# Performance work log

Measured on AMD Instinct MI355X. Metric: run time of the kernel, lower is better.

Reference implementation:

```python
import jax, jax.numpy as jnp
import numpy as np

N_QUBITS = 12
MAX_LAYERS = 21
Q_DEPTH = 20
DIM = 2 ** N_QUBITS  # 4096
Q_DELTA = 0.01


def setup_inputs() -> dict:
    key = jax.random.key(0)
    k1, k2 = jax.random.split(key)
    return {
        "input_features": jax.random.normal(k1, (4096, 2048), dtype=jnp.float32),
        "q_params": Q_DELTA * jax.random.normal(k2, (MAX_LAYERS * N_QUBITS,), dtype=jnp.float32),
    }


def _cnot(state, c, t):
    # state: (B, 2,2,...,2); flip target axis where control bit == 1
    s0, s1 = jnp.split(state, 2, axis=c + 1)
    s1 = jnp.flip(s1, axis=t + 1)
    return jnp.concatenate([s0, s1], axis=c + 1)


def _ry(state, theta, w):
    # real RY rotation: [[cos(t/2), -sin(t/2)], [sin(t/2), cos(t/2)]]
    s0, s1 = jnp.split(state, 2, axis=w + 1)
    c = jnp.cos(theta * 0.5)
    s = jnp.sin(theta * 0.5)
    return jnp.concatenate([c * s0 - s * s1, s * s0 + c * s1], axis=w + 1)


def _entangling_layer(state):
    for i in range(0, N_QUBITS - 1, 2):
        state = _cnot(state, i, i + 1)
    for i in range(1, N_QUBITS - 1, 2):
        state = _cnot(state, i, i + 1)
    return state


def _forward(input_features, q_params):
    q_in = jnp.tanh(input_features) * (np.pi / 2.0)
    B, F = q_in.shape
    # AmplitudeEmbedding: pad with 0.5 to 2^n, then L2-normalize
    padded = jnp.concatenate(
        [q_in, jnp.full((B, DIM - F), 0.5, dtype=q_in.dtype)], axis=1
    )
    state = padded / jnp.linalg.norm(padded, axis=1, keepdims=True)
    state = state.reshape((B,) + (2,) * N_QUBITS)  # qubit 0 = most significant axis

    weights = q_params.reshape(MAX_LAYERS, N_QUBITS)

    @jax.checkpoint
    def layer(st, theta):
        st = _entangling_layer(st)
        for j in range(N_QUBITS):
            st = _ry(st, theta[j], j)
        return st, None

    state, _ = jax.lax.scan(layer, state, weights[1:1 + Q_DEPTH])

    probs = jnp.square(state.reshape(B, DIM))  # (B, 4096)
    bit_pos = N_QUBITS - 1 - jnp.arange(N_QUBITS)
    bits = (jnp.arange(DIM)[:, None] >> bit_pos[None, :]) & 1  # (DIM, 12)
    signs = (1.0 - 2.0 * bits).astype(probs.dtype)
    return probs @ signs  # (B, 12) expvals of PauliZ per qubit


def reference(input_features, q_params):
    return _forward(input_features, q_params)
```

## Files before the change

### kernel.cpp

```cpp
#include <hip/hip_runtime.h>
#include <math.h>

#define LAYERS 20
#define CS_FLOATS 480

typedef float f2 __attribute__((ext_vector_type(2)));

__global__ void cs_precompute(const float* __restrict__ qp, float* __restrict__ cs) {
    int i = threadIdx.x;
    if (i < 240) {
        float t = 0.5f * qp[12 + i];
        cs[2 * i]     = cosf(t);
        cs[2 * i + 1] = sinf(t);
    }
}

#define S0 u0.x
#define S1 u0.y
#define S2 u1.x
#define S3 u1.y
#define S4 u2.x
#define S5 u2.y
#define S6 u3.x
#define S7 u3.y
#define S8 u4.x
#define S9 u4.y
#define S10 u5.x
#define S11 u5.y
#define S12 u6.x
#define S13 u6.y
#define S14 u7.x
#define S15 u7.y
#define S16 u8.x
#define S17 u8.y
#define S18 u9.x
#define S19 u9.y
#define S20 u10.x
#define S21 u10.y
#define S22 u11.x
#define S23 u11.y
#define S24 u12.x
#define S25 u12.y
#define S26 u13.x
#define S27 u13.y
#define S28 u14.x
#define S29 u14.y
#define S30 u15.x
#define S31 u15.y

#define ALL16(F) F(0) F(1) F(2) F(3) F(4) F(5) F(6) F(7) F(8) F(9) F(10) F(11) \
  F(12) F(13) F(14) F(15)
#define ALL32S(F) F(0) F(1) F(2) F(3) F(4) F(5) F(6) F(7) F(8) F(9) F(10) F(11) \
  F(12) F(13) F(14) F(15) F(16) F(17) F(18) F(19) F(20) F(21) F(22) F(23) \
  F(24) F(25) F(26) F(27) F(28) F(29) F(30) F(31)

#define KQ1(F) F(0,8) F(1,9) F(2,10) F(3,11) F(4,12) F(5,13) F(6,14) F(7,15)
#define KQ2(F) F(0,4) F(1,5) F(2,6) F(3,7) F(8,12) F(9,13) F(10,14) F(11,15)
#define KQ3(F) F(0,2) F(1,3) F(4,6) F(5,7) F(8,10) F(9,11) F(12,14) F(13,15)
#define KQ4(F) F(0,1) F(2,3) F(4,5) F(6,7) F(8,9) F(10,11) F(12,13) F(14,15)

#define P16(F) F(0,16) F(1,17) F(2,18) F(3,19) F(4,20) F(5,21) F(6,22) F(7,23) \
  F(8,24) F(9,25) F(10,26) F(11,27) F(12,28) F(13,29) F(14,30) F(15,31)
#define P8(F) F(0,8) F(1,9) F(2,10) F(3,11) F(4,12) F(5,13) F(6,14) F(7,15) \
  F(16,24) F(17,25) F(18,26) F(19,27) F(20,28) F(21,29) F(22,30) F(23,31)
#define P4(F) F(0,4) F(1,5) F(2,6) F(3,7) F(8,12) F(9,13) F(10,14) F(11,15) \
  F(16,20) F(17,21) F(18,22) F(19,23) F(24,28) F(25,29) F(26,30) F(27,31)
#define P2(F) F(0,2) F(1,3) F(4,6) F(5,7) F(8,10) F(9,11) F(12,14) F(13,15) \
  F(16,18) F(17,19) F(20,22) F(21,23) F(24,26) F(25,27) F(28,30) F(29,31)
#define P1(F) F(0,1) F(2,3) F(4,5) F(6,7) F(8,9) F(10,11) F(12,13) F(14,15) \
  F(16,17) F(18,19) F(20,21) F(22,23) F(24,25) F(26,27) F(28,29) F(30,31)

#define XA16(F) F(0) F(1) F(2) F(3) F(4) F(5) F(6) F(7)
#define XB16(F) F(8) F(9) F(10) F(11) F(12) F(13) F(14) F(15)

template <int CTRL>
__device__ __forceinline__ float dppf(float x) {
    return __int_as_float(__builtin_amdgcn_mov_dpp(
        __float_as_int(x), CTRL, 0xF, 0xF, true));
}
template <int IMM>
__device__ __forceinline__ float swzf(float x) {
    return __int_as_float(__builtin_amdgcn_ds_swizzle(__float_as_int(x), IMM));
}

template <bool PRE>
__global__ __launch_bounds__(128)
void qsim(const float* __restrict__ feats,
          const float* __restrict__ qp,
          const float* __restrict__ cs,
          float* __restrict__ out)
{
    __shared__ f2 xch2[2 * 64 * 9];
    float* xchf = (float*)xch2;

    const int tid  = threadIdx.x;
    const int lane = tid & 63;
    const int w    = tid >> 6;
    const int row  = blockIdx.x;

    const int sl0     = lane ^ (lane >> 1) ^ ((lane >> 2) & 5);
    const int addr0   = sl0 << 2;
    const int addr1   = (sl0 ^ 48) << 2;
    const int addrX32 = (lane ^ 32) << 2;

    const int mybase = w * 576 + lane * 9;
    const int pbase  = (1 - w) * 576 + lane * 9;

#define DCLU(k) f2 u##k;
    ALL16(DCLU)
#undef DCLU

    const float* fr = feats + (size_t)row * 2048;
    if (w == 0) {
        float fsum = 0.f;
#define LD(r) { float x_ = tanhf(fr[((r) << 6) + lane]) * 1.5707963267948966f; \
                S##r = x_; fsum += x_ * x_; }
        ALL32S(LD)
#undef LD
#pragma unroll
        for (int m = 32; m >= 1; m >>= 1) fsum += __shfl_xor(fsum, m, 64);
        if (lane == 0) xchf[0] = fsum;
    }
    __syncthreads();
    const float inv = rsqrtf(xchf[0] + 512.0f);
    __syncthreads();
    if (w == 0) {
#define SC(k) u##k *= inv;
        ALL16(SC)
#undef SC
    } else {
        const float padv = 0.5f * inv;
        const f2 pv2 = {padv, padv};
#define PD(k) u##k = pv2;
        ALL16(PD)
#undef PD
    }

#pragma unroll 1
    for (int l = 0; l < LAYERS; ++l) {
        const float* csl = cs + l * 24;

#define BPV(a, x) __int_as_float(__builtin_amdgcn_ds_bpermute( \
                      (((a) & 1) ? addr1 : addr0), __float_as_int(x)))
#define FIX(a) S##a = BPV(a, S##a);
#define C2(a,b) { float t_ = S##a; S##a = BPV(a, S##b); S##b = BPV(b, t_); }
#define C4(a,b,c,d) { float t_ = S##a; S##a = BPV(a, S##b); \
        S##b = BPV(b, S##c); S##c = BPV(c, S##d); S##d = BPV(d, t_); }
#define C8(a,b,c,d,e,f,g,h) { float t_ = S##a; S##a = BPV(a, S##b); \
        S##b = BPV(b, S##c); S##c = BPV(c, S##d); S##d = BPV(d, S##e); \
        S##e = BPV(e, S##f); S##f = BPV(f, S##g); S##g = BPV(g, S##h); \
        S##h = BPV(h, t_); }
        if (w == 0) {
            FIX(0) FIX(1)
            C2(2, 3)
            C4(4, 7, 5, 6)
            C4(8, 12, 11, 14)
            C4(9, 13, 10, 15)
            C8(16, 28, 23, 25, 17, 29, 22, 24)
            C8(18, 31, 21, 26, 19, 30, 20, 27)
        } else {
            C8(0, 16, 12, 27, 2, 19, 14, 24)
            C8(1, 17, 13, 26, 3, 18, 15, 25)
            C8(4, 23, 9, 29, 6, 20, 11, 30)
            C8(5, 22, 8, 28, 7, 21, 10, 31)
        }
#undef BPV
#undef FIX
#undef C2
#undef C4
#undef C8

#define RYPK(a,b) { f2 A_ = u##a, B_ = u##b; \
        u##a = c_ * A_ - s_ * B_; u##b = s_ * A_ + c_ * B_; }
#define RYREGK(J, LIST) { float c_, s_; \
        if constexpr (PRE) { c_ = csl[2*(J)]; s_ = csl[2*(J)+1]; } \
        else { float t_ = 0.5f * qp[12 + l*12 + (J)]; __sincosf(t_, &s_, &c_); } \
        LIST(RYPK) }
        RYREGK(1, KQ1)
        RYREGK(2, KQ2)
        RYREGK(3, KQ3)
        RYREGK(4, KQ4)
#undef RYREGK
#undef RYPK

        {
            float c_, s_;
            if constexpr (PRE) { c_ = csl[10]; s_ = csl[11]; }
            else { float t_ = 0.5f * qp[12 + l*12 + 5]; __sincosf(t_, &s_, &c_); }
            const f2 ss5_ = {-s_, s_};
#define Q5(k) { f2 sw_ = u##k.yx; u##k = c_ * u##k + ss5_ * sw_; }
            ALL16(Q5)
#undef Q5
        }

        {
            float c_, s_, ssel_;
#define GETCS(jj) \
            if constexpr (PRE) { c_ = csl[12 + 2*(jj)]; s_ = csl[13 + 2*(jj)]; } \
            else { float t_ = 0.5f * qp[12 + l*12 + 6 + (jj)]; __sincosf(t_, &s_, &c_); }
#define LQ(k, EX) { f2 p_; p_.x = EX(u##k.x); p_.y = EX(u##k.y); \
                    u##k = c_ * u##k + ssel_ * p_; }

            GETCS(0); ssel_ = (lane & 32) ? s_ : -s_;
#define EX6(x) __int_as_float(__builtin_amdgcn_ds_bpermute(addrX32, __float_as_int(x)))
#define LQ6(k) LQ(k, EX6)
            ALL16(LQ6)
#undef LQ6
#undef EX6
            GETCS(1); ssel_ = (lane & 16) ? s_ : -s_;
#define LQ7(k) LQ(k, swzf<0x401F>)
            ALL16(LQ7)
#undef LQ7
            GETCS(2); ssel_ = (lane & 8) ? s_ : -s_;
#define LQ8(k) LQ(k, dppf<0x128>)
            ALL16(LQ8)
#undef LQ8
            GETCS(3); ssel_ = (lane & 4) ? s_ : -s_;
#define LQ9(k) LQ(k, swzf<0x101F>)
            ALL16(LQ9)
#undef LQ9
            GETCS(4); ssel_ = (lane & 2) ? s_ : -s_;
#define LQ10(k) LQ(k, dppf<0x4E>)
            ALL16(LQ10)
#undef LQ10
            GETCS(5); ssel_ = (lane & 1) ? s_ : -s_;
#define LQ11(k) LQ(k, dppf<0xB1>)
            ALL16(LQ11)
#undef LQ11
#undef LQ
#undef GETCS
        }

        {
            float c0_, s0_;
            if constexpr (PRE) { c0_ = csl[0]; s0_ = csl[1]; }
            else { float t_ = 0.5f * qp[12 + l*12]; __sincosf(t_, &s0_, &c0_); }
            const float ssel0_ = w ? s0_ : -s0_;
#define XWA(k) xch2[mybase + (k)] = u##k;
#define XRA(k) { f2 p_ = xch2[pbase + (k)]; u##k = c0_ * u##k + ssel0_ * p_; }
#define XWB(k) xch2[mybase + ((k) - 8)] = u##k;
#define XRB(k) { f2 p_ = xch2[pbase + ((k) - 8)]; u##k = c0_ * u##k + ssel0_ * p_; }
            XA16(XWA)
            __syncthreads();
            XA16(XRA)
            __syncthreads();
            XB16(XWB)
            __syncthreads();
            XB16(XRB)
            __syncthreads();
#undef XWA
#undef XRA
#undef XWB
#undef XRB
        }
    }

    float T = 0.f;
#define SQT(k) u##k *= u##k; T += u##k.x + u##k.y;
    ALL16(SQT)
#undef SQT

    float part[12];
    part[0] = w ? -T : T;
#define ADDB(a,b) + S##b
    { float S;
      S = 0.f P16(ADDB); part[1] = T - 2.f * S;
      S = 0.f P8(ADDB);  part[2] = T - 2.f * S;
      S = 0.f P4(ADDB);  part[3] = T - 2.f * S;
      S = 0.f P2(ADDB);  part[4] = T - 2.f * S;
      S = 0.f P1(ADDB);  part[5] = T - 2.f * S; }
#undef ADDB
#pragma unroll
    for (int q = 6; q < 12; ++q) {
        const int m = 32 >> (q - 6);
        part[q] = (lane & m) ? -T : T;
    }
#pragma unroll
    for (int q = 0; q < 12; ++q) {
#pragma unroll
        for (int m2 = 32; m2 >= 1; m2 >>= 1) part[q] += __shfl_xor(part[q], m2, 64);
    }
    if (lane == 0) {
#pragma unroll
        for (int q = 0; q < 12; ++q) xchf[w * 12 + q] = part[q];
    }
    __syncthreads();
    if (tid < 12) out[row * 12 + tid] = xchf[tid] + xchf[12 + tid];
}

extern "C" void kernel_launch(void* const* d_in, const int* in_sizes, int n_in,
                              void* d_out, int out_size, void* d_ws, size_t ws_size,
                              hipStream_t stream) {
    (void)in_sizes; (void)n_in; (void)out_size;
    const float* feats = (const float*)d_in[0];
    const float* qp    = (const float*)d_in[1];
    float* out = (float*)d_out;

    if (ws_size >= CS_FLOATS * sizeof(float)) {
        float* cs = (float*)d_ws;
        cs_precompute<<<1, 256, 0, stream>>>(qp, cs);
        qsim<true><<<4096, 128, 0, stream>>>(feats, qp, cs, out);
    } else {
        qsim<false><<<4096, 128, 0, stream>>>(feats, qp, nullptr, out);
    }
}
```

Before: 316.9 us.

## Use packed FMA asm, permlane32 swap, and single-phase LDS exchange

Replaces the vector f2 arithmetic in the RY rotations with explicit v_pk_mul/v_pk_fma inline asm, including an op_sel variant that handles the in-register swap for qubit 5. The cross-half-wave exchange for qubit 6 moves from ds_bpermute to the permlane32_swap builtin, avoiding an LDS round trip. The qubit-0 exchange between the two waves now writes all 16 registers at once into a larger shared buffer, cutting four barriers per layer to two. The trade is more LDS per block, which may affect occupancy, and inline asm that limits the compiler's scheduling.

```diff
diff --git a/kernel.cpp b/kernel.cpp
--- a/kernel.cpp
+++ b/kernel.cpp
@@ -70,8 +70,22 @@
 #define P1(F) F(0,1) F(2,3) F(4,5) F(6,7) F(8,9) F(10,11) F(12,13) F(14,15) \
   F(16,17) F(18,19) F(20,21) F(22,23) F(24,25) F(26,27) F(28,29) F(30,31)
 
-#define XA16(F) F(0) F(1) F(2) F(3) F(4) F(5) F(6) F(7)
-#define XB16(F) F(8) F(9) F(10) F(11) F(12) F(13) F(14) F(15)
+__device__ __forceinline__ f2 pk_mul(f2 a, f2 b) {
+    f2 d;
+    asm("v_pk_mul_f32 %0, %1, %2" : "=v"(d) : "v"(a), "v"(b));
+    return d;
+}
+__device__ __forceinline__ f2 pk_fma(f2 a, f2 b, f2 c) {
+    f2 d;
+    asm("v_pk_fma_f32 %0, %1, %2, %3" : "=v"(d) : "v"(a), "v"(b), "v"(c));
+    return d;
+}
+__device__ __forceinline__ f2 pk_fma_sw1(f2 a, f2 b, f2 c) {
+    f2 d;
+    asm("v_pk_fma_f32 %0, %1, %2, %3 op_sel:[0,1,0] op_sel_hi:[1,0,1]"
+        : "=v"(d) : "v"(a), "v"(b), "v"(c));
+    return d;
+}
 
 template <int CTRL>
 __device__ __forceinline__ float dppf(float x) {
@@ -90,7 +104,7 @@
           const float* __restrict__ cs,
           float* __restrict__ out)
 {
-    __shared__ f2 xch2[2 * 64 * 9];
+    __shared__ f2 xch2[2 * 64 * 17];
     float* xchf = (float*)xch2;
 
     const int tid  = threadIdx.x;
@@ -98,13 +112,12 @@
     const int w    = tid >> 6;
     const int row  = blockIdx.x;
 
-    const int sl0     = lane ^ (lane >> 1) ^ ((lane >> 2) & 5);
-    const int addr0   = sl0 << 2;
-    const int addr1   = (sl0 ^ 48) << 2;
-    const int addrX32 = (lane ^ 32) << 2;
-
-    const int mybase = w * 576 + lane * 9;
-    const int pbase  = (1 - w) * 576 + lane * 9;
+    const int sl0   = lane ^ (lane >> 1) ^ ((lane >> 2) & 5);
+    const int addr0 = sl0 << 2;
+    const int addr1 = (sl0 ^ 48) << 2;
+
+    const int mybase = w * 1088 + lane * 17;
+    const int pbase  = (1 - w) * 1088 + lane * 17;
 
 #define DCLU(k) f2 u##k;
     ALL16(DCLU)
@@ -118,7 +131,7 @@
         ALL32S(LD)
 #undef LD
 #pragma unroll
-        for (int m = 32; m >= 1; m >>= 1) fsum += __shfl_xor(fsum, m, 64);
+    for (int m = 32; m >= 1; m >>= 1) fsum += __shfl_xor(fsum, m, 64);
         if (lane == 0) xchf[0] = fsum;
     }
     __syncthreads();
@@ -171,10 +184,12 @@
 #undef C8
 
 #define RYPK(a,b) { f2 A_ = u##a, B_ = u##b; \
-        u##a = c_ * A_ - s_ * B_; u##b = s_ * A_ + c_ * B_; }
+        u##a = pk_fma(cc_, A_, pk_mul(ns_, B_)); \
+        u##b = pk_fma(ss_, A_, pk_mul(cc_, B_)); }
 #define RYREGK(J, LIST) { float c_, s_; \
         if constexpr (PRE) { c_ = csl[2*(J)]; s_ = csl[2*(J)+1]; } \
         else { float t_ = 0.5f * qp[12 + l*12 + (J)]; __sincosf(t_, &s_, &c_); } \
+        const f2 cc_ = {c_, c_}, ss_ = {s_, s_}, ns_ = {-s_, -s_}; \
         LIST(RYPK) }
         RYREGK(1, KQ1)
         RYREGK(2, KQ2)
@@ -187,8 +202,8 @@
             float c_, s_;
             if constexpr (PRE) { c_ = csl[10]; s_ = csl[11]; }
             else { float t_ = 0.5f * qp[12 + l*12 + 5]; __sincosf(t_, &s_, &c_); }
-            const f2 ss5_ = {-s_, s_};
-#define Q5(k) { f2 sw_ = u##k.yx; u##k = c_ * u##k + ss5_ * sw_; }
+            const f2 cc_ = {c_, c_}, ss5_ = {-s_, s_};
+#define Q5(k) u##k = pk_fma_sw1(ss5_, u##k, pk_mul(cc_, u##k));
             ALL16(Q5)
 #undef Q5
         }
@@ -199,10 +214,13 @@
             if constexpr (PRE) { c_ = csl[12 + 2*(jj)]; s_ = csl[13 + 2*(jj)]; } \
             else { float t_ = 0.5f * qp[12 + l*12 + 6 + (jj)]; __sincosf(t_, &s_, &c_); }
 #define LQ(k, EX) { f2 p_; p_.x = EX(u##k.x); p_.y = EX(u##k.y); \
-                    u##k = c_ * u##k + ssel_ * p_; }
+                    const f2 sl_ = {ssel_, ssel_}, cc_ = {c_, c_}; \
+                    u##k = pk_fma(cc_, u##k, pk_mul(sl_, p_)); }
 
             GETCS(0); ssel_ = (lane & 32) ? s_ : -s_;
-#define EX6(x) __int_as_float(__builtin_amdgcn_ds_bpermute(addrX32, __float_as_int(x)))
+#define EX6(x) ({ auto pr_ = __builtin_amdgcn_permlane32_swap( \
+                      __float_as_int(x), __float_as_int(x), false, false); \
+                  __int_as_float((lane & 32) ? pr_[0] : pr_[1]); })
 #define LQ6(k) LQ(k, EX6)
             ALL16(LQ6)
 #undef LQ6
@@ -236,22 +254,16 @@
             if constexpr (PRE) { c0_ = csl[0]; s0_ = csl[1]; }
             else { float t_ = 0.5f * qp[12 + l*12]; __sincosf(t_, &s0_, &c0_); }
             const float ssel0_ = w ? s0_ : -s0_;
-#define XWA(k) xch2[mybase + (k)] = u##k;
-#define XRA(k) { f2 p_ = xch2[pbase + (k)]; u##k = c0_ * u##k + ssel0_ * p_; }
-#define XWB(k) xch2[mybase + ((k) - 8)] = u##k;
-#define XRB(k) { f2 p_ = xch2[pbase + ((k) - 8)]; u##k = c0_ * u##k + ssel0_ * p_; }
-            XA16(XWA)
+            const f2 cc0_ = {c0_, c0_}, sl0_ = {ssel0_, ssel0_};
+#define XW(k) xch2[mybase + (k)] = u##k;
+#define XR(k) { f2 p_ = xch2[pbase + (k)]; \
+                u##k = pk_fma(cc0_, u##k, pk_mul(sl0_, p_)); }
+            ALL16(XW)
             __syncthreads();
-            XA16(XRA)
+            ALL16(XR)
             __syncthreads();
-            XB16(XWB)
-            __syncthreads();
-            XB16(XRB)
-            __syncthreads();
-#undef XWA
-#undef XRA
-#undef XWB
-#undef XRB
+#undef XW
+#undef XR
         }
     }
 
```

Result: slower. 354.5 us (+11.8%).

## Use three-shear rotations for in-register qubits and pack two rows per block

Applied to the files above, without the earlier changes.

Register-resident RY rotations for qubits 1-5 now use a three-shear (tan/sin) form, three FMAs per pair, with the per-layer -tan(phi/2) and sin(phi) precomputed. Qubit 5 is now handled the same way instead of by a swizzle on packed pairs. Lane-level rotations now run on scalar registers rather than packed f2 values. Each block now processes two rows (256 threads, doubled shared exchange buffer), which halves the block count and may cut per-block overhead, at the cost of block-wide barriers shared between the two rows.

```diff
diff --git a/kernel.cpp b/kernel.cpp
--- a/kernel.cpp
+++ b/kernel.cpp
@@ -9,9 +9,15 @@
 __global__ void cs_precompute(const float* __restrict__ qp, float* __restrict__ cs) {
     int i = threadIdx.x;
     if (i < 240) {
-        float t = 0.5f * qp[12 + i];
-        cs[2 * i]     = cosf(t);
-        cs[2 * i + 1] = sinf(t);
+        int j = i % 12;
+        float phi = 0.5f * qp[12 + i];
+        if (j >= 1 && j <= 5) {
+            cs[2 * i]     = -tanf(0.5f * phi);
+            cs[2 * i + 1] = sinf(phi);
+        } else {
+            cs[2 * i]     = cosf(phi);
+            cs[2 * i + 1] = sinf(phi);
+        }
     }
 }
 
@@ -54,11 +60,6 @@
   F(12) F(13) F(14) F(15) F(16) F(17) F(18) F(19) F(20) F(21) F(22) F(23) \
   F(24) F(25) F(26) F(27) F(28) F(29) F(30) F(31)
 
-#define KQ1(F) F(0,8) F(1,9) F(2,10) F(3,11) F(4,12) F(5,13) F(6,14) F(7,15)
-#define KQ2(F) F(0,4) F(1,5) F(2,6) F(3,7) F(8,12) F(9,13) F(10,14) F(11,15)
-#define KQ3(F) F(0,2) F(1,3) F(4,6) F(5,7) F(8,10) F(9,11) F(12,14) F(13,15)
-#define KQ4(F) F(0,1) F(2,3) F(4,5) F(6,7) F(8,9) F(10,11) F(12,13) F(14,15)
-
 #define P16(F) F(0,16) F(1,17) F(2,18) F(3,19) F(4,20) F(5,21) F(6,22) F(7,23) \
   F(8,24) F(9,25) F(10,26) F(11,27) F(12,28) F(13,29) F(14,30) F(15,31)
 #define P8(F) F(0,8) F(1,9) F(2,10) F(3,11) F(4,12) F(5,13) F(6,14) F(7,15) \
@@ -84,27 +85,28 @@
 }
 
 template <bool PRE>
-__global__ __launch_bounds__(128)
+__global__ __launch_bounds__(256)
 void qsim(const float* __restrict__ feats,
           const float* __restrict__ qp,
           const float* __restrict__ cs,
           float* __restrict__ out)
 {
-    __shared__ f2 xch2[2 * 64 * 9];
+    __shared__ f2 xch2[2 * 2 * 64 * 9];
     float* xchf = (float*)xch2;
 
-    const int tid  = threadIdx.x;
-    const int lane = tid & 63;
-    const int w    = tid >> 6;
-    const int row  = blockIdx.x;
+    const int tid    = threadIdx.x;
+    const int lane   = tid & 63;
+    const int w      = (tid >> 6) & 1;
+    const int pairid = tid >> 7;
+    const int row    = blockIdx.x * 2 + pairid;
 
     const int sl0     = lane ^ (lane >> 1) ^ ((lane >> 2) & 5);
     const int addr0   = sl0 << 2;
     const int addr1   = (sl0 ^ 48) << 2;
     const int addrX32 = (lane ^ 32) << 2;
 
-    const int mybase = w * 576 + lane * 9;
-    const int pbase  = (1 - w) * 576 + lane * 9;
+    const int mybase = pairid * 1152 + w * 576 + lane * 9;
+    const int pbase  = pairid * 1152 + (1 - w) * 576 + lane * 9;
 
 #define DCLU(k) f2 u##k;
     ALL16(DCLU)
@@ -119,10 +121,10 @@
 #undef LD
 #pragma unroll
         for (int m = 32; m >= 1; m >>= 1) fsum += __shfl_xor(fsum, m, 64);
-        if (lane == 0) xchf[0] = fsum;
+        if (lane == 0) xchf[pairid] = fsum;
     }
     __syncthreads();
-    const float inv = rsqrtf(xchf[0] + 512.0f);
+    const float inv = rsqrtf(xchf[pairid] + 512.0f);
     __syncthreads();
     if (w == 0) {
 #define SC(k) u##k *= inv;
@@ -170,64 +172,54 @@
 #undef C4
 #undef C8
 
-#define RYPK(a,b) { f2 A_ = u##a, B_ = u##b; \
-        u##a = c_ * A_ - s_ * B_; u##b = s_ * A_ + c_ * B_; }
-#define RYREGK(J, LIST) { float c_, s_; \
-        if constexpr (PRE) { c_ = csl[2*(J)]; s_ = csl[2*(J)+1]; } \
-        else { float t_ = 0.5f * qp[12 + l*12 + (J)]; __sincosf(t_, &s_, &c_); } \
-        LIST(RYPK) }
-        RYREGK(1, KQ1)
-        RYREGK(2, KQ2)
-        RYREGK(3, KQ3)
-        RYREGK(4, KQ4)
-#undef RYREGK
-#undef RYPK
-
-        {
-            float c_, s_;
-            if constexpr (PRE) { c_ = csl[10]; s_ = csl[11]; }
-            else { float t_ = 0.5f * qp[12 + l*12 + 5]; __sincosf(t_, &s_, &c_); }
-            const f2 ss5_ = {-s_, s_};
-#define Q5(k) { f2 sw_ = u##k.yx; u##k = c_ * u##k + ss5_ * sw_; }
-            ALL16(Q5)
-#undef Q5
-        }
+#define SHP(a,b) { S##a = fmaf(nt_, S##b, S##a); \
+                   S##b = fmaf(s_,  S##a, S##b); \
+                   S##a = fmaf(nt_, S##b, S##a); }
+#define SHREG(J, LIST) { float nt_, s_; \
+        if constexpr (PRE) { nt_ = csl[2*(J)]; s_ = csl[2*(J)+1]; } \
+        else { float p_ = 0.5f * qp[12 + l*12 + (J)]; \
+               s_ = __sinf(p_); nt_ = -__tanf(0.5f * p_); } \
+        LIST(SHP) }
+        SHREG(1, P16)
+        SHREG(2, P8)
+        SHREG(3, P4)
+        SHREG(4, P2)
+        SHREG(5, P1)
+#undef SHREG
+#undef SHP
 
         {
             float c_, s_, ssel_;
 #define GETCS(jj) \
             if constexpr (PRE) { c_ = csl[12 + 2*(jj)]; s_ = csl[13 + 2*(jj)]; } \
             else { float t_ = 0.5f * qp[12 + l*12 + 6 + (jj)]; __sincosf(t_, &s_, &c_); }
-#define LQ(k, EX) { f2 p_; p_.x = EX(u##k.x); p_.y = EX(u##k.y); \
-                    u##k = c_ * u##k + ssel_ * p_; }
 
             GETCS(0); ssel_ = (lane & 32) ? s_ : -s_;
-#define EX6(x) __int_as_float(__builtin_amdgcn_ds_bpermute(addrX32, __float_as_int(x)))
-#define LQ6(k) LQ(k, EX6)
-            ALL16(LQ6)
-#undef LQ6
-#undef EX6
+#define LRYS(r) { float p_ = __int_as_float(__builtin_amdgcn_ds_bpermute( \
+                      addrX32, __float_as_int(S##r))); \
+                  S##r = c_ * S##r + ssel_ * p_; }
+            ALL32S(LRYS)
+#undef LRYS
             GETCS(1); ssel_ = (lane & 16) ? s_ : -s_;
-#define LQ7(k) LQ(k, swzf<0x401F>)
-            ALL16(LQ7)
-#undef LQ7
+#define LRYS(r) { float p_ = swzf<0x401F>(S##r); S##r = c_ * S##r + ssel_ * p_; }
+            ALL32S(LRYS)
+#undef LRYS
             GETCS(2); ssel_ = (lane & 8) ? s_ : -s_;
-#define LQ8(k) LQ(k, dppf<0x128>)
-            ALL16(LQ8)
-#undef LQ8
+#define LRYS(r) { float p_ = dppf<0x128>(S##r); S##r = c_ * S##r + ssel_ * p_; }
+            ALL32S(LRYS)
+#undef LRYS
             GETCS(3); ssel_ = (lane & 4) ? s_ : -s_;
-#define LQ9(k) LQ(k, swzf<0x101F>)
-            ALL16(LQ9)
-#undef LQ9
+#define LRYS(r) { float p_ = swzf<0x101F>(S##r); S##r = c_ * S##r + ssel_ * p_; }
+            ALL32S(LRYS)
+#undef LRYS
             GETCS(4); ssel_ = (lane & 2) ? s_ : -s_;
-#define LQ10(k) LQ(k, dppf<0x4E>)
-            ALL16(LQ10)
-#undef LQ10
+#define LRYS(r) { float p_ = dppf<0x4E>(S##r); S##r = c_ * S##r + ssel_ * p_; }
+            ALL32S(LRYS)
+#undef LRYS
             GETCS(5); ssel_ = (lane & 1) ? s_ : -s_;
-#define LQ11(k) LQ(k, dppf<0xB1>)
-            ALL16(LQ11)
-#undef LQ11
-#undef LQ
+#define LRYS(r) { float p_ = dppf<0xB1>(S##r); S##r = c_ * S##r + ssel_ * p_; }
+            ALL32S(LRYS)
+#undef LRYS
 #undef GETCS
         }
 
@@ -282,10 +274,14 @@
     }
     if (lane == 0) {
 #pragma unroll
-        for (int q = 0; q < 12; ++q) xchf[w * 12 + q] = part[q];
+        for (int q = 0; q < 12; ++q) xchf[pairid * 24 + w * 12 + q] = part[q];
     }
     __syncthreads();
-    if (tid < 12) out[row * 12 + tid] = xchf[tid] + xchf[12 + tid];
+    if (tid < 24) {
+        const int pr = tid / 12, q = tid - pr * 12;
+        out[(blockIdx.x * 2 + pr) * 12 + q] =
+            xchf[pr * 24 + q] + xchf[pr * 24 + 12 + q];
+    }
 }
 
 extern "C" void kernel_launch(void* const* d_in, const int* in_sizes, int n_in,
@@ -299,8 +295,8 @@
     if (ws_size >= CS_FLOATS * sizeof(float)) {
         float* cs = (float*)d_ws;
         cs_precompute<<<1, 256, 0, stream>>>(qp, cs);
-        qsim<true><<<4096, 128, 0, stream>>>(feats, qp, cs, out);
+        qsim<true><<<2048, 256, 0, stream>>>(feats, qp, cs, out);
     } else {
-        qsim<false><<<4096, 128, 0, stream>>>(feats, qp, nullptr, out);
-    }
-}
+        qsim<false><<<2048, 256, 0, stream>>>(feats, qp, nullptr, out);
+    }
+}
```

New measurement: 336.5 us. 6.2% more time.
